# Performance work log

Measured on AMD Instinct MI355X. Metric: run time of the kernel, lower is better.

The kernel has to match this reference:

```python
import jax, jax.numpy as jnp
import numpy as np
import math

HID, NH, NKV, HD = 2048, 16, 4, 128
GROUPS = NH // NKV

def fq(x, bits, axis=None):
    # symmetric fake-quant with straight-through rounding; per-tensor unless axis given
    qmax = 2.0 ** (bits - 1) - 1.0
    if axis is None:
        amax = jnp.max(jnp.abs(x))
    else:
        amax = jnp.max(jnp.abs(x), axis=axis, keepdims=True)
    scale = jnp.maximum(amax, 1e-8) / qmax
    q = jnp.clip(jnp.round(x / scale), -qmax - 1.0, qmax) * scale
    return x + jax.lax.stop_gradient(q - x)

def dyn_quant_linear(x, W, b, w_bits=8):
    # DynamicQuantLinear: per-out-channel weight fake-quant + dynamic per-tensor 8-bit act quant
    Wq = fq(W, w_bits, axis=1)          # W: [out, in]
    xq = fq(x, 8)
    y = xq @ Wq.T
    return y + b if b is not None else y

def fq_matmul(a, b, a_bits, b_bits):
    # FakeQuantMatmul
    return jnp.einsum('hqd,hdk->hqk', fq(a, a_bits), fq(b, b_bits))

def rotate_half(x):
    x1, x2 = jnp.split(x, 2, axis=-1)
    return jnp.concatenate([-x2, x1], axis=-1)

def setup_inputs() -> dict:
    key = jax.random.key(0)
    ks = jax.random.split(key, 12)
    inp = {
        'hidden_states': jax.random.normal(ks[0], (1, 512, HID), jnp.float32),
        'cos': jax.random.uniform(ks[1], (1, 512, HD), jnp.float32),
        'sin': jax.random.uniform(ks[2], (1, 512, HD), jnp.float32),
        'cache_k': jax.random.normal(ks[3], (NKV, 8192, HD), jnp.float32),
        'cache_v': jax.random.normal(ks[4], (NKV, 8192, HD), jnp.float32),
        'mask': jnp.zeros((1, 512, 8192), jnp.float32),
        'Wq': jax.random.normal(ks[5], (NH * HD, HID), jnp.float32) * 0.02,
        'bq': jnp.zeros((NH * HD,), jnp.float32),
        'Wk': jax.random.normal(ks[6], (NKV * HD, HID), jnp.float32) * 0.02,
        'bk': jnp.zeros((NKV * HD,), jnp.float32),
        'Wv': jax.random.normal(ks[7], (NKV * HD, HID), jnp.float32) * 0.02,
        'bv': jnp.zeros((NKV * HD,), jnp.float32),
        'Wo': jax.random.normal(ks[8], (HID, NH * HD), jnp.float32) * 0.02,
    }
    return inp

def reference(hidden_states, cos, sin, cache_k, cache_v, mask, Wq, bq, Wk, bk, Wv, bv, Wo):
    # ConstFakeQuant on incoming caches
    cache_k = fq(cache_k, 8)
    cache_v = fq(cache_v, 8)
    seqlen = hidden_states.shape[1]
    x = hidden_states.reshape(seqlen, HID)  # batch_size == 1
    q = dyn_quant_linear(x, Wq, bq).reshape(seqlen, NH, HD).transpose(1, 0, 2)    # [NH,S,D]
    k = dyn_quant_linear(x, Wk, bk).reshape(seqlen, NKV, HD).transpose(1, 0, 2)   # [NKV,S,D]
    v = dyn_quant_linear(x, Wv, bv).reshape(seqlen, NKV, HD).transpose(1, 0, 2)   # [NKV,S,D]
    # RoPE
    q = q * cos + rotate_half(q) * sin
    k = k * cos + rotate_half(k) * sin
    c_len = cache_k.shape[1]
    # sliding KV cache: drop oldest seqlen, append new
    cache_k = jnp.concatenate([cache_k[:, seqlen:, :], k], axis=1)   # [NKV,c_len,D]
    cache_v = jnp.concatenate([cache_v[:, seqlen:, :], v], axis=1)
    kT = cache_k.transpose(0, 2, 1)                                   # [NKV,D,c_len]
    q4 = q.reshape(NKV, GROUPS * seqlen, HD)
    attn = fq_matmul(q4, kT, 8, 8)                                    # [NKV,G*S,c_len]
    attn = attn.reshape(NH, seqlen, c_len) / math.sqrt(HD)
    attn = attn + mask
    attn = jax.nn.softmax(attn, axis=-1)
    attn = attn.reshape(NKV, GROUPS * seqlen, c_len)
    out = fq_matmul(attn, cache_v, 8, 8)                              # sv: [NKV,G*S,D]
    out = out.reshape(NH, seqlen, HD).transpose(1, 0, 2).reshape(1, seqlen, HID)
    out = dyn_quant_linear(out.reshape(seqlen, HID), Wo, None).reshape(1, seqlen, HID)
    # cache outputs re-fake-quantized
    k_out = fq(k, 8)
    v_out = fq(v, 8)
    return (out, k_out, v_out)
```

## Files before the change

kernel.cpp:

```cpp
#include <hip/hip_runtime.h>
#include <math.h>

#define S_LEN 512
#define HID 2048
#define NH 16
#define NKV 4
#define HD 128
#define CL 8192
#define TAILN (CL - S_LEN)
#define NKO (NKV * S_LEN * HD)
#define KS1 16
#define KCH1 (CL / KS1)
#define KS2 4
#define KCH2 (CL / KS2)
#define INV_SQRT_HD 0.08838834764831845f

typedef unsigned short u16;
typedef __attribute__((ext_vector_type(8))) unsigned short u16x8;
typedef __attribute__((ext_vector_type(4))) unsigned short u16x4;
typedef __attribute__((ext_vector_type(8))) short bf16x8;
typedef __attribute__((ext_vector_type(4))) float f32x4;

enum {
  SC_AMAX_X = 0, SC_AMAX_CK, SC_AMAX_CK_TAIL, SC_AMAX_CV, SC_AMAX_CV_TAIL,
  SC_AMAX_Q, SC_AMAX_K, SC_AMAX_V, SC_AMAX_AO, SC_MIN_L,
  SC_NUM
};

__device__ __forceinline__ float warpMax64(float v) {
  #pragma unroll
  for (int o = 32; o; o >>= 1) v = fmaxf(v, __shfl_down(v, o, 64));
  return v;
}
__device__ __forceinline__ float warpMin64(float v) {
  #pragma unroll
  for (int o = 32; o; o >>= 1) v = fminf(v, __shfl_down(v, o, 64));
  return v;
}
__device__ __forceinline__ float blockMax256(float v) {
  __shared__ float sm_[4];
  __syncthreads();
  v = warpMax64(v);
  if ((threadIdx.x & 63) == 0) sm_[threadIdx.x >> 6] = v;
  __syncthreads();
  return fmaxf(fmaxf(sm_[0], sm_[1]), fmaxf(sm_[2], sm_[3]));
}
__device__ __forceinline__ float blockMin256(float v) {
  __shared__ float sn_[4];
  __syncthreads();
  v = warpMin64(v);
  if ((threadIdx.x & 63) == 0) sn_[threadIdx.x >> 6] = v;
  __syncthreads();
  return fminf(fminf(sn_[0], sn_[1]), fminf(sn_[2], sn_[3]));
}
__device__ __forceinline__ void atomicMinPosF(float* a, float v) {
  atomicMin((unsigned int*)a, __float_as_uint(v));
}
__device__ __forceinline__ float clampq(float q) {
  return fminf(fmaxf(q, -128.f), 127.f);
}
__device__ __forceinline__ u16 bf16bits(float f) {
  return (u16)(__float_as_uint(f) >> 16);
}
__device__ __forceinline__ float mk_scale(float am) {
  return fmaxf(am, 1e-8f) / 127.f;
}
__device__ __forceinline__ void gl2lds16(const u16* g, u16* l) {
  __builtin_amdgcn_global_load_lds((const __attribute__((address_space(1))) void*)g,
                                   (__attribute__((address_space(3))) void*)l, 16, 0, 0);
}

__global__ __launch_bounds__(256) void k_pre(const float* __restrict__ hidden,
                                             const float* __restrict__ ck, const float* __restrict__ cv,
                                             float* __restrict__ pp) {
  int b = blockIdx.x, tid = threadIdx.x;
  if (b < 512) {
    const int n4 = S_LEN * HID / 4;
    float m = 0.f;
    const float4* x4 = (const float4*)hidden;
    for (int i = b * 256 + tid; i < n4; i += 512 * 256) {
      float4 v = x4[i];
      m = fmaxf(m, fmaxf(fmaxf(fabsf(v.x), fabsf(v.y)), fmaxf(fabsf(v.z), fabsf(v.w))));
    }
    m = blockMax256(m);
    if (tid == 0) pp[b] = m;
  } else {
    int isv = b >= 1024;
    int bb = b - (isv ? 1024 : 512);
    const float4* x4 = (const float4*)(isv ? cv : ck);
    const int n4 = NKV * CL * HD / 4;
    float mf = 0.f, mt = 0.f;
    for (int i = bb * 256 + tid; i < n4; i += 512 * 256) {
      float4 v = x4[i];
      float a = fmaxf(fmaxf(fabsf(v.x), fabsf(v.y)), fmaxf(fabsf(v.z), fabsf(v.w)));
      mf = fmaxf(mf, a);
      int t = (i >> 5) & (CL - 1);
      if (t >= S_LEN) mt = fmaxf(mt, a);
    }
    mf = blockMax256(mf);
    mt = blockMax256(mt);
    if (tid == 0) {
      pp[512 + isv * 1024 + bb] = mf;
      pp[1024 + isv * 1024 + bb] = mt;
    }
  }
}

__global__ __launch_bounds__(256) void k_reduce_pre(const float* __restrict__ pp, float* __restrict__ sc) {
  const int slots[5] = {SC_AMAX_X, SC_AMAX_CK, SC_AMAX_CK_TAIL, SC_AMAX_CV, SC_AMAX_CV_TAIL};
  if (threadIdx.x == 0) sc[SC_MIN_L] = INFINITY;
  #pragma unroll
  for (int r = 0; r < 5; r++) {
    float v = fmaxf(pp[r * 512 + threadIdx.x], pp[r * 512 + 256 + threadIdx.x]);
    v = blockMax256(v);
    if (threadIdx.x == 0) sc[slots[r]] = v;
  }
}

__global__ __launch_bounds__(256) void k_quant_w_all(const float* __restrict__ Wq, const float* __restrict__ Wk,
                                                     const float* __restrict__ Wv, const float* __restrict__ Wo,
                                                     u16* __restrict__ WQb, u16* __restrict__ WKb,
                                                     u16* __restrict__ WVb, u16* __restrict__ WOb,
                                                     float* __restrict__ SWq, float* __restrict__ SWk,
                                                     float* __restrict__ SWv, float* __restrict__ SWo) {
  int r = blockIdx.x;
  const float* W; u16* Wb; float* SW; int row;
  if (r < 2048)      { W = Wq; Wb = WQb; SW = SWq; row = r; }
  else if (r < 2560) { W = Wk; Wb = WKb; SW = SWk; row = r - 2048; }
  else if (r < 3072) { W = Wv; Wb = WVb; SW = SWv; row = r - 2560; }
  else               { W = Wo; Wb = WOb; SW = SWo; row = r - 3072; }
  size_t base = (size_t)row * HID;
  const float4* w4 = (const float4*)(W + base);
  int tid = threadIdx.x;
  float4 va = w4[tid];
  float4 vb = w4[tid + 256];
  float am = fmaxf(fmaxf(fmaxf(fabsf(va.x), fabsf(va.y)), fmaxf(fabsf(va.z), fabsf(va.w))),
                   fmaxf(fmaxf(fabsf(vb.x), fabsf(vb.y)), fmaxf(fabsf(vb.z), fabsf(vb.w))));
  am = blockMax256(am);
  float s = fmaxf(am, 1e-8f) / 127.f;
  if (tid == 0) SW[row] = s;
  u16x4 oa, ob;
  oa[0] = bf16bits(clampq(rintf(va.x / s)));
  oa[1] = bf16bits(clampq(rintf(va.y / s)));
  oa[2] = bf16bits(clampq(rintf(va.z / s)));
  oa[3] = bf16bits(clampq(rintf(va.w / s)));
  ob[0] = bf16bits(clampq(rintf(vb.x / s)));
  ob[1] = bf16bits(clampq(rintf(vb.y / s)));
  ob[2] = bf16bits(clampq(rintf(vb.z / s)));
  ob[3] = bf16bits(clampq(rintf(vb.w / s)));
  *(u16x4*)(Wb + base + (size_t)tid * 4) = oa;
  *(u16x4*)(Wb + base + (size_t)(tid + 256) * 4) = ob;
}

__global__ __launch_bounds__(256) void k_quant_act_b(const float* __restrict__ in, u16* __restrict__ outp,
                                                     int n4, const float* __restrict__ sc, int axslot) {
  float s = mk_scale(sc[axslot]);
  const float4* i4 = (const float4*)in;
  for (int i = blockIdx.x * 256 + threadIdx.x; i < n4; i += gridDim.x * 256) {
    float4 v = i4[i];
    u16x4 o;
    o[0] = bf16bits(clampq(rintf(v.x / s)));
    o[1] = bf16bits(clampq(rintf(v.y / s)));
    o[2] = bf16bits(clampq(rintf(v.z / s)));
    o[3] = bf16bits(clampq(rintf(v.w / s)));
    *(u16x4*)(outp + (size_t)i * 4) = o;
  }
}

__global__ __launch_bounds__(256) void k_quant_q(const float* __restrict__ QB, u16* __restrict__ QI,
                                                 const float* __restrict__ sc) {
  int idx = blockIdx.x * 256 + threadIdx.x;
  float s = mk_scale(sc[SC_AMAX_Q]);
  int e = idx * 4;
  int srow = e >> 11, rem = e & 2047;
  int h = rem >> 7, d = rem & 127;
  float4 v = *(const float4*)&QB[e];
  u16x4 o;
  o[0] = bf16bits(clampq(rintf(v.x / s)));
  o[1] = bf16bits(clampq(rintf(v.y / s)));
  o[2] = bf16bits(clampq(rintf(v.z / s)));
  o[3] = bf16bits(clampq(rintf(v.w / s)));
  *(u16x4*)(QI + ((size_t)h * S_LEN + srow) * HD + d) = o;
}

#define GQ_STAGE(BUF, K0)                                                          \
  {                                                                                \
    _Pragma("unroll")                                                              \
    for (int i = 0; i < 2; i++) {                                                  \
      int b = tid + i * 256;                                                       \
      int row = b >> 3, c8d = b & 7, c8s = c8d ^ (row & 7);                        \
      gl2lds16(A + (size_t)(r0 + row) * HID + (K0) + c8s * 8, Al[BUF] + b * 8);    \
    }                                                                              \
    _Pragma("unroll")                                                              \
    for (int i = 0; i < 2; i++) {                                                  \
      int b = tid + i * 256;                                                       \
      int row = b >> 3, c8d = b & 7, c8s = c8d ^ (row & 7);                        \
      gl2lds16(B + (size_t)(c0 + row) * HID + (K0) + c8s * 8, Bl[BUF] + b * 8);    \
    }                                                                              \
  }

#define GQ_TILE(BUF)                                                               \
  {                                                                                \
    _Pragma("unroll")                                                              \
    for (int ks = 0; ks < 2; ks++) {                                               \
      bf16x8 af[2], bfr[2];                                                        \
      _Pragma("unroll")                                                            \
      for (int a = 0; a < 2; a++) {                                                \
        int row = wy * 32 + a * 16 + c;                                            \
        af[a] = *(const bf16x8*)(Al[BUF] + row * 64 + (((4 * ks + g) ^ (row & 7)) * 8)); \
      }                                                                            \
      _Pragma("unroll")                                                            \
      for (int b2 = 0; b2 < 2; b2++) {                                             \
        int row = wx * 32 + b2 * 16 + c;                                           \
        bfr[b2] = *(const bf16x8*)(Bl[BUF] + row * 64 + (((4 * ks + g) ^ (row & 7)) * 8)); \
      }                                                                            \
      _Pragma("unroll")                                                            \
      for (int a = 0; a < 2; a++)                                                  \
        _Pragma("unroll")                                                          \
        for (int b2 = 0; b2 < 2; b2++)                                             \
          acc[a][b2] = __builtin_amdgcn_mfma_f32_16x16x32_bf16(af[a], bfr[b2], acc[a][b2], 0, 0, 0); \
    }                                                                              \
  }

__global__ __launch_bounds__(256) void k_gemm_qkv(const u16* __restrict__ A,
                                                  const u16* __restrict__ WQb, const u16* __restrict__ WKb,
                                                  const u16* __restrict__ WVb,
                                                  const float* __restrict__ SWq, const float* __restrict__ SWk,
                                                  const float* __restrict__ SWv,
                                                  const float* __restrict__ bq, const float* __restrict__ bk,
                                                  const float* __restrict__ bv,
                                                  const float* __restrict__ sc,
                                                  float* __restrict__ QB, float* __restrict__ KB,
                                                  float* __restrict__ VB) {
  __shared__ u16 Al[2][64 * 64];
  __shared__ u16 Bl[2][64 * 64];
  int bx = blockIdx.x;
  const u16* B; const float* SW; const float* bias; float* C; int N, c0;
  if (bx < 32)      { B = WQb; SW = SWq; bias = bq; C = QB; N = HID; c0 = bx * 64; }
  else if (bx < 40) { B = WKb; SW = SWk; bias = bk; C = KB; N = NKV * HD; c0 = (bx - 32) * 64; }
  else              { B = WVb; SW = SWv; bias = bv; C = VB; N = NKV * HD; c0 = (bx - 40) * 64; }
  int tid = threadIdx.x, lane = tid & 63, w = tid >> 6;
  int g = lane >> 4, c = lane & 15;
  int wy = w >> 1, wx = w & 1;
  int r0 = blockIdx.y * 64;
  float sx = mk_scale(sc[SC_AMAX_X]);
  f32x4 acc[2][2] = {};
  GQ_STAGE(0, 0)
  __syncthreads();
  for (int k0 = 0; k0 < HID; k0 += 128) {
    GQ_STAGE(1, k0 + 64)
    GQ_TILE(0)
    __syncthreads();
    if (k0 + 128 < HID) GQ_STAGE(0, k0 + 128)
    GQ_TILE(1)
    __syncthreads();
  }
  #pragma unroll
  for (int a = 0; a < 2; a++)
    #pragma unroll
    for (int b2 = 0; b2 < 2; b2++) {
      int col = c0 + wx * 32 + b2 * 16 + c;
      float sca = sx * SW[col];
      float bs = bias[col];
      #pragma unroll
      for (int r = 0; r < 4; r++) {
        int row = r0 + wy * 32 + a * 16 + 4 * g + r;
        C[(size_t)row * N + col] = acc[a][b2][r] * sca + bs;
      }
    }
}

__global__ __launch_bounds__(256) void k_gemm_q(const u16* __restrict__ A, const u16* __restrict__ B,
                                                const float* __restrict__ SW, const float* __restrict__ sc,
                                                int axslot, float* __restrict__ C, int M, int N, int K) {
  __shared__ u16 Al[2][64 * 64];
  __shared__ u16 Bl[2][64 * 64];
  int tid = threadIdx.x, lane = tid & 63, w = tid >> 6;
  int g = lane >> 4, c = lane & 15;
  int wy = w >> 1, wx = w & 1;
  int r0 = blockIdx.y * 64, c0 = blockIdx.x * 64;
  float sx = mk_scale(sc[axslot]);
  f32x4 acc[2][2] = {};
  GQ_STAGE(0, 0)
  __syncthreads();
  for (int k0 = 0; k0 < HID; k0 += 128) {
    GQ_STAGE(1, k0 + 64)
    GQ_TILE(0)
    __syncthreads();
    if (k0 + 128 < HID) GQ_STAGE(0, k0 + 128)
    GQ_TILE(1)
    __syncthreads();
  }
  #pragma unroll
  for (int a = 0; a < 2; a++)
    #pragma unroll
    for (int b2 = 0; b2 < 2; b2++) {
      int col = c0 + wx * 32 + b2 * 16 + c;
      float sca = sx * SW[col];
      #pragma unroll
      for (int r = 0; r < 4; r++) {
        int row = r0 + wy * 32 + a * 16 + 4 * g + r;
        C[(size_t)row * N + col] = acc[a][b2][r] * sca;
      }
    }
}

__global__ __launch_bounds__(256) void k_rope_amax(float* __restrict__ QB, float* __restrict__ KB,
                                                   const float* __restrict__ VB,
                                                   const float* __restrict__ cosb, const float* __restrict__ sinb,
                                                   float* __restrict__ PR) {
  const int nQ = S_LEN * NH * 64;
  const int nK = S_LEN * NKV * 64;
  int idx = blockIdx.x * 256 + threadIdx.x;
  float am = 0.f;
  if (idx < nQ) {
    int s = idx >> 10, rem = idx & 1023, h = rem >> 6, d = rem & 63;
    float c1 = cosb[s * HD + d], s1 = sinb[s * HD + d];
    float c2 = cosb[s * HD + d + 64], s2 = sinb[s * HD + d + 64];
    float* p = &QB[(size_t)s * (NH * HD) + h * HD + d];
    float x1 = p[0], x2 = p[64];
    float y1 = x1 * c1 - x2 * s1;
    float y2 = x2 * c2 + x1 * s2;
    p[0] = y1; p[64] = y2;
    am = fmaxf(fabsf(y1), fabsf(y2));
  } else if (idx < nQ + nK) {
    int j = idx - nQ;
    int s = j >> 8, rem = j & 255, h = rem >> 6, d = rem & 63;
    float c1 = cosb[s * HD + d], s1 = sinb[s * HD + d];
    float c2 = cosb[s * HD + d + 64], s2 = sinb[s * HD + d + 64];
    float* p = &KB[(size_t)s * (NKV * HD) + h * HD + d];
    float x1 = p[0], x2 = p[64];
    float y1 = x1 * c1 - x2 * s1;
    float y2 = x2 * c2 + x1 * s2;
    p[0] = y1; p[64] = y2;
    am = fmaxf(fabsf(y1), fabsf(y2));
  } else {
    int j = idx - nQ - nK;
    float4 v = ((const float4*)VB)[j];
    am = fmaxf(fmaxf(fabsf(v.x), fabsf(v.y)), fmaxf(fabsf(v.z), fabsf(v.w)));
  }
  am = blockMax256(am);
  if (threadIdx.x == 0) PR[blockIdx.x] = am;
}

__global__ __launch_bounds__(256) void k_reduce_rope(const float* __restrict__ PR, float* __restrict__ sc) {
  float v = 0.f;
  #pragma unroll
  for (int i = 0; i < 8; i++) v = fmaxf(v, PR[threadIdx.x + 256 * i]);
  v = blockMax256(v);
  if (threadIdx.x == 0) sc[SC_AMAX_Q] = v;
  v = fmaxf(PR[2048 + threadIdx.x], PR[2048 + 256 + threadIdx.x]);
  v = blockMax256(v);
  if (threadIdx.x == 0) sc[SC_AMAX_K] = v;
  v = PR[2560 + threadIdx.x];
  v = blockMax256(v);
  if (threadIdx.x == 0) sc[SC_AMAX_V] = v;
}

__global__ __launch_bounds__(256) void k_build_cache2(const float* __restrict__ ck, const float* __restrict__ cv,
                                                      const float* __restrict__ KB, const float* __restrict__ VB,
                                                      u16* __restrict__ KCb, u16* __restrict__ VCb,
                                                      u16* __restrict__ VT, float* __restrict__ dout,
                                                      const float* __restrict__ sc) {
  __shared__ u16 T[64][140];
  int b = blockIdx.x;
  int isv = b >= NKV * 128;
  int bb = b - isv * NKV * 128;
  int kvh = bb >> 7, tb = bb & 127;
  float s1 = mk_scale(sc[isv ? SC_AMAX_CV : SC_AMAX_CK]);
  float tq = fminf(rintf(sc[isv ? SC_AMAX_CV_TAIL : SC_AMAX_CK_TAIL] / s1), 127.f) * s1;
  float s2 = fmaxf(fmaxf(tq, sc[isv ? SC_AMAX_V : SC_AMAX_K]), 1e-8f) / 127.f;
  float so = mk_scale(sc[isv ? SC_AMAX_V : SC_AMAX_K]);
  const float* cache = isv ? cv : ck;
  const float* fresh = isv ? VB : KB;
  u16* Cb = isv ? VCb : KCb;
  int tid = threadIdx.x;
  int t0 = tb * 64;
  #pragma unroll
  for (int i = 0; i < 8; i++) {
    int idx = tid + i * 256;
    int t = idx >> 5, d4 = (idx & 31) << 2;
    int tt = t0 + t;
    float4 x;
    float q0_, q1_, q2_, q3_;
    if (tt < TAILN) {
      x = *(const float4*)&cache[((size_t)kvh * CL + tt + S_LEN) * HD + d4];
      q0_ = clampq(rintf(clampq(rintf(x.x / s1)) * s1 / s2));
      q1_ = clampq(rintf(clampq(rintf(x.y / s1)) * s1 / s2));
      q2_ = clampq(rintf(clampq(rintf(x.z / s1)) * s1 / s2));
      q3_ = clampq(rintf(clampq(rintf(x.w / s1)) * s1 / s2));
    } else {
      x = *(const float4*)&fresh[(size_t)(tt - TAILN) * (NKV * HD) + kvh * HD + d4];
      q0_ = clampq(rintf(x.x / s2));
      q1_ = clampq(rintf(x.y / s2));
      q2_ = clampq(rintf(x.z / s2));
      q3_ = clampq(rintf(x.w / s2));
      float4 o;
      o.x = clampq(rintf(x.x / so)) * so;
      o.y = clampq(rintf(x.y / so)) * so;
      o.z = clampq(rintf(x.z / so)) * so;
      o.w = clampq(rintf(x.w / so)) * so;
      *(float4*)&dout[(size_t)S_LEN * HID + (size_t)isv * NKO +
                      ((size_t)kvh * S_LEN + (tt - TAILN)) * HD + d4] = o;
    }
    u16x4 ov;
    ov[0] = bf16bits(q0_); ov[1] = bf16bits(q1_); ov[2] = bf16bits(q2_); ov[3] = bf16bits(q3_);
    *(u16x4*)(Cb + ((size_t)kvh * CL + tt) * HD + d4) = ov;
    if (isv) *(u16x4*)&T[t][d4] = ov;
  }
  if (isv) {
    __syncthreads();
    #pragma unroll
    for (int i = 0; i < 4; i++) {
      int j = tid + i * 256;
      int d = j >> 3, tc = (j & 7) << 3;
      u16x8 v;
      #pragma unroll
      for (int k = 0; k < 8; k++) v[k] = T[tc + k][d];
      *(u16x8*)(VT + ((size_t)kvh * HD + d) * CL + t0 + tc) = v;
    }
  }
}

#define M1_STAGE(BUF, KBASE)                                                       \
  {                                                                                \
    const u16* kgt = Kg + (size_t)(KBASE) * HD;                                    \
    _Pragma("unroll")                                                              \
    for (int i = 0; i < 4; i++) {                                                  \
      int b = tid + i * 256;                                                       \
      int row = b >> 4, c8d = b & 15, c8s = c8d ^ (row & 7);                       \
      gl2lds16(kgt + row * HD + c8s * 8, Kl[BUF] + b * 8);                         \
    }                                                                              \
  }

#define M1_TILE(BUF, KBASE)                                                        \
  {                                                                                \
    const int kbase_ = (KBASE);                                                    \
    f32x4 sc4[4];                                                                  \
    _Pragma("unroll")                                                              \
    for (int kf = 0; kf < 4; kf++) {                                               \
      f32x4 s4 = {0.f, 0.f, 0.f, 0.f};                                             \
      int krow = kf * 16 + c;                                                      \
      _Pragma("unroll")                                                            \
      for (int ds = 0; ds < 4; ds++) {                                             \
        bf16x8 kf8 = *(const bf16x8*)(Kl[BUF] + krow * HD + (((4 * ds + g) ^ (krow & 7)) * 8)); \
        s4 = __builtin_amdgcn_mfma_f32_16x16x32_bf16(qf[ds], kf8, s4, 0, 0, 0);    \
      }                                                                            \
      sc4[kf] = s4;                                                                \
    }                                                                              \
    _Pragma("unroll")                                                              \
    for (int r = 0; r < 4; r++) {                                                  \
      float v0 = fmaf(sc4[0][r], sscale, mrb[r * CL + kbase_ + c]);                \
      float v1 = fmaf(sc4[1][r], sscale, mrb[r * CL + kbase_ + 16 + c]);           \
      float v2 = fmaf(sc4[2][r], sscale, mrb[r * CL + kbase_ + 32 + c]);           \
      float v3 = fmaf(sc4[3][r], sscale, mrb[r * CL + kbase_ + 48 + c]);           \
      float tmax = fmaxf(fmaxf(v0, v1), fmaxf(v2, v3));                            \
      float nm = fmaxf(m[r], tmax);                                                \
      float e0 = __expf(v0 - nm), e1 = __expf(v1 - nm);                            \
      float e2 = __expf(v2 - nm), e3 = __expf(v3 - nm);                            \
      float f = __expf(m[r] - nm);                                                 \
      l[r] = fmaf(l[r], f, (e0 + e1) + (e2 + e3));                                 \
      m[r] = nm;                                                                   \
    }                                                                              \
  }

__global__ __launch_bounds__(256) void k_mattn1(const u16* __restrict__ QI, const u16* __restrict__ KCb,
                                                const float* __restrict__ mask, const float* __restrict__ sc,
                                                float* __restrict__ PM, float* __restrict__ PL) {
  __shared__ u16 Kl[2][64 * HD];
  int bid = blockIdx.x;
  int wki = (bid & 7) * (NH * 8 * KS1 / 8) + (bid >> 3);
  int kc = wki >> 7, rem2 = wki & 127, qb = rem2 >> 4, h = rem2 & 15, kv = h >> 2;
  int tid = threadIdx.x, lane = tid & 63, wv = tid >> 6, g = lane >> 4, c = lane & 15;
  float sq  = mk_scale(sc[SC_AMAX_Q]);
  float sck = mk_scale(sc[SC_AMAX_CK]);
  float tqk = fminf(rintf(sc[SC_AMAX_CK_TAIL] / sck), 127.f) * sck;
  float skn = fmaxf(fmaxf(tqk, sc[SC_AMAX_K]), 1e-8f) / 127.f;
  float sscale = sq * skn * INV_SQRT_HD;
  int q0 = qb * 64 + wv * 16;
  bf16x8 qf[4];
  {
    const u16* qrow = QI + ((size_t)h * S_LEN + q0 + c) * HD + g * 8;
    #pragma unroll
    for (int ds = 0; ds < 4; ds++) qf[ds] = *(const bf16x8*)(qrow + 32 * ds);
  }
  float m[4], l[4];
  #pragma unroll
  for (int r = 0; r < 4; r++) { m[r] = -INFINITY; l[r] = 0.f; }
  int qlane = q0 + 4 * g;
  int kbase0 = kc * KCH1;
  const u16* Kg = KCb + (size_t)kv * CL * HD;
  const float* mrb = mask + (size_t)qlane * CL;
  M1_STAGE(0, kbase0)
  __syncthreads();
  for (int kb = 0; kb < KCH1; kb += 128) {
    M1_STAGE(1, kbase0 + kb + 64)
    M1_TILE(0, kbase0 + kb)
    __syncthreads();
    if (kb + 128 < KCH1) M1_STAGE(0, kbase0 + kb + 128)
    M1_TILE(1, kbase0 + kb + 64)
    __syncthreads();
  }
  #pragma unroll
  for (int r = 0; r < 4; r++) {
    #pragma unroll
    for (int off = 1; off < 16; off <<= 1) {
      float om = __shfl_xor(m[r], off, 64);
      float ol = __shfl_xor(l[r], off, 64);
      float nm = fmaxf(m[r], om);
      l[r] = l[r] * __expf(m[r] - nm) + ol * __expf(om - nm);
      m[r] = nm;
    }
  }
  if (c == 0) {
    size_t base = ((size_t)kc * NH + h) * S_LEN + qlane;
    #pragma unroll
    for (int r = 0; r < 4; r++) { PM[base + r] = m[r]; PL[base + r] = l[r]; }
  }
}

__global__ __launch_bounds__(256) void k_merge4(const float* __restrict__ PM, const float* __restrict__ PL,
                                                float* __restrict__ MLm, float* __restrict__ MLl, float* sc) {
  int idx = blockIdx.x * 256 + threadIdx.x;
  const int st = NH * S_LEN;
  float m = PM[idx];
  #pragma unroll
  for (int p = 1; p < KS1; p++) m = fmaxf(m, PM[p * st + idx]);
  float l = 0.f;
  #pragma unroll
  for (int p = 0; p < KS1; p++) l += PL[p * st + idx] * __expf(PM[p * st + idx] - m);
  MLm[idx] = m; MLl[idx] = l;
  float lm = blockMin256(l);
  if (threadIdx.x == 0) atomicMinPosF(&sc[SC_MIN_L], lm);
}

#define M2_STAGE(BUF, KBASE)                                                       \
  {                                                                                \
    const u16* kgt = Kg + (size_t)(KBASE) * HD;                                    \
    const u16* vgt = Vg + (KBASE);                                                 \
    _Pragma("unroll")                                                              \
    for (int i = 0; i < 4; i++) {                                                  \
      int b = tid + i * 256;                                                       \
      int row = b >> 4, c8d = b & 15, c8s = c8d ^ (row & 7);                       \
      gl2lds16(kgt + row * HD + c8s * 8, Kl[BUF] + b * 8);                         \
    }                                                                              \
    _Pragma("unroll")                                                              \
    for (int i = 0; i < 4; i++) {                                                  \
      int b = tid + i * 256;                                                       \
      int row = b >> 3, c8d = b & 7, c8s = c8d ^ (row & 7);                        \
      gl2lds16(vgt + (size_t)row * CL + c8s * 8, Vl[BUF] + b * 8);                 \
    }                                                                              \
  }

#define M2_TILE(BUF, KBASE)                                                        \
  {                                                                                \
    const int kbase_ = (KBASE);                                                    \
    _Pragma("unroll")                                                              \
    for (int kf = 0; kf < 4; kf++) {                                               \
      f32x4 s4 = {0.f, 0.f, 0.f, 0.f};                                             \
      int krow = kf * 16 + c;                                                      \
      _Pragma("unroll")                                                            \
      for (int ds = 0; ds < 4; ds++) {                                             \
        bf16x8 kf8 = *(const bf16x8*)(Kl[BUF] + krow * HD + (((4 * ds + g) ^ (krow & 7)) * 8)); \
        s4 = __builtin_amdgcn_mfma_f32_16x16x32_bf16(qf[ds], kf8, s4, 0, 0, 0);    \
      }                                                                            \
      _Pragma("unroll")                                                            \
      for (int r = 0; r < 4; r++) {                                                \
        float v = fmaf(s4[r], sscale, mrb[r * CL + kbase_ + kf * 16 + c]);         \
        float pi = fminf(rintf(__expf(v - mreg[r]) * cvl[r]), 127.f);              \
        int prow = 4 * g + r, pcol = kf * 16 + c;                                  \
        Pw[prow * 64 + (pcol ^ ((prow & 7) << 3))] = bf16bits(pi);                 \
      }                                                                            \
    }                                                                              \
    asm volatile("s_waitcnt lgkmcnt(0)" ::: "memory");                             \
    __builtin_amdgcn_sched_barrier(0);                                             \
    bf16x8 pa0 = *(const bf16x8*)(Pw + c * 64 + ((8 * g) ^ ((c & 7) << 3)));       \
    bf16x8 pa1 = *(const bf16x8*)(Pw + c * 64 + ((32 + 8 * g) ^ ((c & 7) << 3)));  \
    _Pragma("unroll")                                                              \
    for (int dt = 0; dt < 8; dt++) {                                               \
      int drow = dt * 16 + c;                                                      \
      bf16x8 vf0 = *(const bf16x8*)(Vl[BUF] + drow * 64 + ((g ^ (drow & 7)) * 8)); \
      acc[dt] = __builtin_amdgcn_mfma_f32_16x16x32_bf16(pa0, vf0, acc[dt], 0, 0, 0); \
      bf16x8 vf1 = *(const bf16x8*)(Vl[BUF] + drow * 64 + (((4 + g) ^ (drow & 7)) * 8)); \
      acc[dt] = __builtin_amdgcn_mfma_f32_16x16x32_bf16(pa1, vf1, acc[dt], 0, 0, 0); \
    }                                                                              \
  }

__global__ __launch_bounds__(256) void k_mattn2(const u16* __restrict__ QI, const u16* __restrict__ KCb,
                                                const u16* __restrict__ VT, const float* __restrict__ mask,
                                                const float* __restrict__ sc, const float* __restrict__ MLm,
                                                const float* __restrict__ MLl, float* __restrict__ AOp) {
  __shared__ u16 Kl[2][64 * HD];
  __shared__ u16 Vl[2][HD * 64];
  __shared__ u16 Pl[4 * 16 * 64];
  int bid = blockIdx.x;
  int wki = (bid & 7) * (NH * 8 * KS2 / 8) + (bid >> 3);
  int kc = wki >> 7, rem2 = wki & 127, qb = rem2 >> 4, h = rem2 & 15, kv = h >> 2;
  int tid = threadIdx.x, lane = tid & 63, wv = tid >> 6, g = lane >> 4, c = lane & 15;
  float sq  = mk_scale(sc[SC_AMAX_Q]);
  float sck = mk_scale(sc[SC_AMAX_CK]);
  float tqk = fminf(rintf(sc[SC_AMAX_CK_TAIL] / sck), 127.f) * sck;
  float skn = fmaxf(fmaxf(tqk, sc[SC_AMAX_K]), 1e-8f) / 127.f;
  float sscale = sq * skn * INV_SQRT_HD;
  float scv = mk_scale(sc[SC_AMAX_CV]);
  float tqv = fminf(rintf(sc[SC_AMAX_CV_TAIL] / scv), 127.f) * scv;
  float svn = fmaxf(fmaxf(tqv, sc[SC_AMAX_V]), 1e-8f) / 127.f;
  float sp  = mk_scale(1.0f / sc[SC_MIN_L]);
  float rsp = 1.0f / sp;
  float psv = sp * svn;
  int q0 = qb * 64 + wv * 16;
  bf16x8 qf[4];
  {
    const u16* qrow = QI + ((size_t)h * S_LEN + q0 + c) * HD + g * 8;
    #pragma unroll
    for (int ds = 0; ds < 4; ds++) qf[ds] = *(const bf16x8*)(qrow + 32 * ds);
  }
  int qlane = q0 + 4 * g;
  float mreg[4], cvl[4];
  #pragma unroll
  for (int r = 0; r < 4; r++) {
    mreg[r] = MLm[h * S_LEN + qlane + r];
    cvl[r] = rsp / MLl[h * S_LEN + qlane + r];
  }
  f32x4 acc[8] = {};
  const u16* Kg = KCb + (size_t)kv * CL * HD;
  const u16* Vg = VT + (size_t)kv * HD * CL;
  const float* mrb = mask + (size_t)qlane * CL;
  int kbase0 = kc * KCH2;
  u16* Pw = Pl + wv * 1024;
  M2_STAGE(0, kbase0)
  __syncthreads();
  for (int kb = 0; kb < KCH2; kb += 128) {
    M2_STAGE(1, kbase0 + kb + 64)
    M2_TILE(0, kbase0 + kb)
    __syncthreads();
    if (kb + 128 < KCH2) M2_STAGE(0, kbase0 + kb + 128)
    M2_TILE(1, kbase0 + kb + 64)
    __syncthreads();
  }
  float* outp = AOp + (size_t)kc * S_LEN * HID;
  #pragma unroll
  for (int dt = 0; dt < 8; dt++)
    #pragma unroll
    for (int r = 0; r < 4; r++)
      outp[(size_t)(qlane + r) * HID + h * HD + dt * 16 + c] = acc[dt][r] * psv;
}

__global__ __launch_bounds__(256) void k_combine_ao(const float* __restrict__ AOp, float* __restrict__ AO,
                                                    float* __restrict__ PA) {
  int idx = blockIdx.x * 256 + threadIdx.x;
  const int st = S_LEN * HID / 4;
  const f32x4* p4 = (const f32x4*)AOp;
  f32x4 a = p4[idx];
  #pragma unroll
  for (int p = 1; p < KS2; p++) {
    f32x4 b = p4[p * st + idx];
    a = a + b;
  }
  *((f32x4*)AO + idx) = a;
  float am = fmaxf(fmaxf(fabsf(a[0]), fabsf(a[1])), fmaxf(fabsf(a[2]), fabsf(a[3])));
  am = blockMax256(am);
  if (threadIdx.x == 0) PA[blockIdx.x] = am;
}

__global__ __launch_bounds__(256) void k_reduce_ao(const float* __restrict__ PA, float* __restrict__ sc) {
  float v = 0.f;
  #pragma unroll
  for (int i = 0; i < 4; i++) v = fmaxf(v, PA[threadIdx.x + 256 * i]);
  v = blockMax256(v);
  if (threadIdx.x == 0) sc[SC_AMAX_AO] = v;
}

extern "C" void kernel_launch(void* const* d_in, const int* in_sizes, int n_in,
                              void* d_out, int out_size, void* d_ws, size_t ws_size,
                              hipStream_t stream) {
  const float* hidden = (const float*)d_in[0];
  const float* cosb   = (const float*)d_in[1];
  const float* sinb   = (const float*)d_in[2];
  const float* cachek = (const float*)d_in[3];
  const float* cachev = (const float*)d_in[4];
  const float* mask   = (const float*)d_in[5];
  const float* Wq     = (const float*)d_in[6];
  const float* bq     = (const float*)d_in[7];
  const float* Wk     = (const float*)d_in[8];
  const float* bk     = (const float*)d_in[9];
  const float* Wv     = (const float*)d_in[10];
  const float* bv     = (const float*)d_in[11];
  const float* Wo     = (const float*)d_in[12];
  float* out = (float*)d_out;

  char* base = (char*)d_ws;
  auto alloc = [&](size_t bytes) { char* p = base; base += (bytes + 255) & ~(size_t)255; return p; };

  float* SC  = (float*)alloc(64 * 4);
  float* PP  = (float*)alloc(2560 * 4);
  float* PR  = (float*)alloc(2816 * 4);
  float* PA  = (float*)alloc(1024 * 4);
  float* SWq = (float*)alloc(HID * 4);
  float* SWk = (float*)alloc(NKV * HD * 4);
  float* SWv = (float*)alloc(NKV * HD * 4);
  float* SWo = (float*)alloc(HID * 4);
  u16* XI    = (u16*)alloc((size_t)S_LEN * HID * 2);
  u16* WQb   = (u16*)alloc((size_t)HID * HID * 2);
  u16* WKb   = (u16*)alloc((size_t)NKV * HD * HID * 2);
  u16* WVb   = (u16*)alloc((size_t)NKV * HD * HID * 2);
  u16* WOb   = (u16*)alloc((size_t)HID * HID * 2);
  float* QB  = (float*)alloc((size_t)S_LEN * HID * 4);
  float* KB  = (float*)alloc((size_t)S_LEN * NKV * HD * 4);
  float* VB  = (float*)alloc((size_t)S_LEN * NKV * HD * 4);
  u16* KCb   = (u16*)alloc((size_t)NKV * CL * HD * 2);
  u16* VCb   = (u16*)alloc((size_t)NKV * CL * HD * 2);
  u16* VT    = (u16*)alloc((size_t)NKV * HD * CL * 2);
  u16* QI    = (u16*)alloc((size_t)NH * S_LEN * HD * 2);
  float* PM  = (float*)alloc((size_t)KS1 * NH * S_LEN * 4);
  float* PL  = (float*)alloc((size_t)KS1 * NH * S_LEN * 4);
  float* MLm = (float*)alloc((size_t)NH * S_LEN * 4);
  float* MLl = (float*)alloc((size_t)NH * S_LEN * 4);
  float* AOp = (float*)alloc((size_t)KS2 * S_LEN * HID * 4);
  float* AO  = (float*)alloc((size_t)S_LEN * HID * 4);
  u16* AOi   = (u16*)alloc((size_t)S_LEN * HID * 2);

  k_pre<<<1536, 256, 0, stream>>>(hidden, cachek, cachev, PP);
  k_reduce_pre<<<1, 256, 0, stream>>>(PP, SC);
  k_quant_w_all<<<5120, 256, 0, stream>>>(Wq, Wk, Wv, Wo, WQb, WKb, WVb, WOb, SWq, SWk, SWv, SWo);
  k_quant_act_b<<<1024, 256, 0, stream>>>(hidden, XI, S_LEN * HID / 4, SC, SC_AMAX_X);
  {
    dim3 g(48, S_LEN / 64);
    k_gemm_qkv<<<g, 256, 0, stream>>>(XI, WQb, WKb, WVb, SWq, SWk, SWv, bq, bk, bv, SC, QB, KB, VB);
  }
  k_rope_amax<<<2816, 256, 0, stream>>>(QB, KB, VB, cosb, sinb, PR);
  k_reduce_rope<<<1, 256, 0, stream>>>(PR, SC);
  k_build_cache2<<<NKV * 128 * 2, 256, 0, stream>>>(cachek, cachev, KB, VB, KCb, VCb, VT, out, SC);
  k_quant_q<<<1024, 256, 0, stream>>>(QB, QI, SC);
  k_mattn1<<<NH * 8 * KS1, 256, 0, stream>>>(QI, KCb, mask, SC, PM, PL);
  k_merge4<<<NH * S_LEN / 256, 256, 0, stream>>>(PM, PL, MLm, MLl, SC);
  k_mattn2<<<NH * 8 * KS2, 256, 0, stream>>>(QI, KCb, VT, mask, SC, MLm, MLl, AOp);
  k_combine_ao<<<1024, 256, 0, stream>>>(AOp, AO, PA);
  k_reduce_ao<<<1, 256, 0, stream>>>(PA, SC);
  k_quant_act_b<<<1024, 256, 0, stream>>>(AO, AOi, S_LEN * HID / 4, SC, SC_AMAX_AO);
  {
    dim3 g(HID / 64, S_LEN / 64);
    k_gemm_q<<<g, 256, 0, stream>>>(AOi, WOb, SWo, SC, SC_AMAX_AO, out, S_LEN, HID, HID);
  }
  (void)in_sizes; (void)n_in; (void)out_size; (void)ws_size;
}
```

Measured before the change: 211.6 us.

## Compute transposed QK^T in mattn2 and pass P through registers via shuffles

The second attention pass now has each wave handle 32 query rows instead of 16, so every K/V tile loaded into LDS feeds twice as many MFMAs. QK^T is computed with swapped operands so each lane holds consecutive keys for one query, and P is packed and rearranged with cross-lane shuffles instead of a round trip through shared memory. The split over keys goes from 4 to 8 chunks to keep the grid size the same. In exchange the kernel uses more registers, since accumulators double, and the combine kernel reads more partial outputs.

```diff
diff --git a/kernel.cpp b/kernel.cpp
--- a/kernel.cpp
+++ b/kernel.cpp
@@ -11,11 +11,12 @@
 #define NKO (NKV * S_LEN * HD)
 #define KS1 16
 #define KCH1 (CL / KS1)
-#define KS2 4
+#define KS2 8
 #define KCH2 (CL / KS2)
 #define INV_SQRT_HD 0.08838834764831845f
 
 typedef unsigned short u16;
+typedef unsigned int u32;
 typedef __attribute__((ext_vector_type(8))) unsigned short u16x8;
 typedef __attribute__((ext_vector_type(4))) unsigned short u16x4;
 typedef __attribute__((ext_vector_type(8))) short bf16x8;
@@ -555,34 +556,62 @@
 #define M2_TILE(BUF, KBASE)                                                        \
   {                                                                                \
     const int kbase_ = (KBASE);                                                    \
+    u32 pw[2][2][4];                  \
     _Pragma("unroll")                                                              \
     for (int kf = 0; kf < 4; kf++) {                                               \
-      f32x4 s4 = {0.f, 0.f, 0.f, 0.f};                                             \
+      f32x4 s40 = {0.f, 0.f, 0.f, 0.f}, s41 = {0.f, 0.f, 0.f, 0.f};                \
       int krow = kf * 16 + c;                                                      \
       _Pragma("unroll")                                                            \
       for (int ds = 0; ds < 4; ds++) {                                             \
         bf16x8 kf8 = *(const bf16x8*)(Kl[BUF] + krow * HD + (((4 * ds + g) ^ (krow & 7)) * 8)); \
-        s4 = __builtin_amdgcn_mfma_f32_16x16x32_bf16(qf[ds], kf8, s4, 0, 0, 0);    \
+        s40 = __builtin_amdgcn_mfma_f32_16x16x32_bf16(kf8, qf[0][ds], s40, 0, 0, 0); \
+        s41 = __builtin_amdgcn_mfma_f32_16x16x32_bf16(kf8, qf[1][ds], s41, 0, 0, 0); \
       }                                                                            \
+      int keyb = kbase_ + kf * 16 + 4 * g;                                         \
+      float p0 = fminf(rintf(__expf(fmaf(s40[0], sscale, mrb0[keyb + 0]) - mreg[0]) * cvl[0]), 127.f); \
+      float p1 = fminf(rintf(__expf(fmaf(s40[1], sscale, mrb0[keyb + 1]) - mreg[0]) * cvl[0]), 127.f); \
+      float p2 = fminf(rintf(__expf(fmaf(s40[2], sscale, mrb0[keyb + 2]) - mreg[0]) * cvl[0]), 127.f); \
+      float p3 = fminf(rintf(__expf(fmaf(s40[3], sscale, mrb0[keyb + 3]) - mreg[0]) * cvl[0]), 127.f); \
+      pw[0][0][kf] = (u32)bf16bits(p0) | ((u32)bf16bits(p1) << 16);                \
+      pw[0][1][kf] = (u32)bf16bits(p2) | ((u32)bf16bits(p3) << 16);                \
+      p0 = fminf(rintf(__expf(fmaf(s41[0], sscale, mrb1[keyb + 0]) - mreg[1]) * cvl[1]), 127.f); \
+      p1 = fminf(rintf(__expf(fmaf(s41[1], sscale, mrb1[keyb + 1]) - mreg[1]) * cvl[1]), 127.f); \
+      p2 = fminf(rintf(__expf(fmaf(s41[2], sscale, mrb1[keyb + 2]) - mreg[1]) * cvl[1]), 127.f); \
+      p3 = fminf(rintf(__expf(fmaf(s41[3], sscale, mrb1[keyb + 3]) - mreg[1]) * cvl[1]), 127.f); \
+      pw[1][0][kf] = (u32)bf16bits(p0) | ((u32)bf16bits(p1) << 16);                \
+      pw[1][1][kf] = (u32)bf16bits(p2) | ((u32)bf16bits(p3) << 16);                \
+    }                                                                              \
+    int src0 = ((g & 1) * 2) * 16 + c;                                             \
+    int src1 = src0 + 16;                                                          \
+    int hi = g >> 1;                                                               \
+    bf16x8 pa[2][2];                                                               \
+    _Pragma("unroll")                                                              \
+    for (int s = 0; s < 2; s++) {                                                  \
       _Pragma("unroll")                                                            \
-      for (int r = 0; r < 4; r++) {                                                \
-        float v = fmaf(s4[r], sscale, mrb[r * CL + kbase_ + kf * 16 + c]);         \
-        float pi = fminf(rintf(__expf(v - mreg[r]) * cvl[r]), 127.f);              \
-        int prow = 4 * g + r, pcol = kf * 16 + c;                                  \
-        Pw[prow * 64 + (pcol ^ ((prow & 7) << 3))] = bf16bits(pi);                 \
+      for (int u = 0; u < 2; u++) {                                                \
+        int a0 = __shfl((int)pw[u][0][2 * s], src0, 64);                           \
+        int b0 = __shfl((int)pw[u][0][2 * s + 1], src0, 64);                       \
+        int a1 = __shfl((int)pw[u][1][2 * s], src0, 64);                           \
+        int b1 = __shfl((int)pw[u][1][2 * s + 1], src0, 64);                       \
+        int a2 = __shfl((int)pw[u][0][2 * s], src1, 64);                           \
+        int b2 = __shfl((int)pw[u][0][2 * s + 1], src1, 64);                       \
+        int a3 = __shfl((int)pw[u][1][2 * s], src1, 64);                           \
+        int b3 = __shfl((int)pw[u][1][2 * s + 1], src1, 64);                       \
+        int4 wv4;                                                                  \
+        wv4.x = hi ? b0 : a0; wv4.y = hi ? b1 : a1;                                \
+        wv4.z = hi ? b2 : a2; wv4.w = hi ? b3 : a3;                                \
+        pa[u][s] = *(bf16x8*)&wv4;                                                 \
       }                                                                            \
     }                                                                              \
-    asm volatile("s_waitcnt lgkmcnt(0)" ::: "memory");                             \
-    __builtin_amdgcn_sched_barrier(0);                                             \
-    bf16x8 pa0 = *(const bf16x8*)(Pw + c * 64 + ((8 * g) ^ ((c & 7) << 3)));       \
-    bf16x8 pa1 = *(const bf16x8*)(Pw + c * 64 + ((32 + 8 * g) ^ ((c & 7) << 3)));  \
     _Pragma("unroll")                                                              \
     for (int dt = 0; dt < 8; dt++) {                                               \
       int drow = dt * 16 + c;                                                      \
       bf16x8 vf0 = *(const bf16x8*)(Vl[BUF] + drow * 64 + ((g ^ (drow & 7)) * 8)); \
-      acc[dt] = __builtin_amdgcn_mfma_f32_16x16x32_bf16(pa0, vf0, acc[dt], 0, 0, 0); \
+      acc[0][dt] = __builtin_amdgcn_mfma_f32_16x16x32_bf16(pa[0][0], vf0, acc[0][dt], 0, 0, 0); \
+      acc[1][dt] = __builtin_amdgcn_mfma_f32_16x16x32_bf16(pa[1][0], vf0, acc[1][dt], 0, 0, 0); \
       bf16x8 vf1 = *(const bf16x8*)(Vl[BUF] + drow * 64 + (((4 + g) ^ (drow & 7)) * 8)); \
-      acc[dt] = __builtin_amdgcn_mfma_f32_16x16x32_bf16(pa1, vf1, acc[dt], 0, 0, 0); \
+      acc[0][dt] = __builtin_amdgcn_mfma_f32_16x16x32_bf16(pa[0][1], vf1, acc[0][dt], 0, 0, 0); \
+      acc[1][dt] = __builtin_amdgcn_mfma_f32_16x16x32_bf16(pa[1][1], vf1, acc[1][dt], 0, 0, 0); \
     }                                                                              \
   }
 
@@ -592,10 +621,9 @@
                                                 const float* __restrict__ MLl, float* __restrict__ AOp) {
   __shared__ u16 Kl[2][64 * HD];
   __shared__ u16 Vl[2][HD * 64];
-  __shared__ u16 Pl[4 * 16 * 64];
   int bid = blockIdx.x;
-  int wki = (bid & 7) * (NH * 8 * KS2 / 8) + (bid >> 3);
-  int kc = wki >> 7, rem2 = wki & 127, qb = rem2 >> 4, h = rem2 & 15, kv = h >> 2;
+  int wki = (bid & 7) * (NH * 4 * KS2 / 8) + (bid >> 3);
+  int kc = wki >> 6, rem2 = wki & 63, qb = rem2 >> 4, h = rem2 & 15, kv = h >> 2;
   int tid = threadIdx.x, lane = tid & 63, wv = tid >> 6, g = lane >> 4, c = lane & 15;
   float sq  = mk_scale(sc[SC_AMAX_Q]);
   float sck = mk_scale(sc[SC_AMAX_CK]);
@@ -608,26 +636,26 @@
   float sp  = mk_scale(1.0f / sc[SC_MIN_L]);
   float rsp = 1.0f / sp;
   float psv = sp * svn;
-  int q0 = qb * 64 + wv * 16;
-  bf16x8 qf[4];
-  {
-    const u16* qrow = QI + ((size_t)h * S_LEN + q0 + c) * HD + g * 8;
+  int q0 = qb * 128 + wv * 32;
+  bf16x8 qf[2][4];
+  #pragma unroll
+  for (int u = 0; u < 2; u++) {
+    const u16* qrow = QI + ((size_t)h * S_LEN + q0 + 16 * u + c) * HD + g * 8;
     #pragma unroll
-    for (int ds = 0; ds < 4; ds++) qf[ds] = *(const bf16x8*)(qrow + 32 * ds);
-  }
-  int qlane = q0 + 4 * g;
-  float mreg[4], cvl[4];
-  #pragma unroll
-  for (int r = 0; r < 4; r++) {
-    mreg[r] = MLm[h * S_LEN + qlane + r];
-    cvl[r] = rsp / MLl[h * S_LEN + qlane + r];
-  }
-  f32x4 acc[8] = {};
+    for (int ds = 0; ds < 4; ds++) qf[u][ds] = *(const bf16x8*)(qrow + 32 * ds);
+  }
+  float mreg[2], cvl[2];
+  #pragma unroll
+  for (int u = 0; u < 2; u++) {
+    mreg[u] = MLm[h * S_LEN + q0 + 16 * u + c];
+    cvl[u] = rsp / MLl[h * S_LEN + q0 + 16 * u + c];
+  }
+  const float* mrb0 = mask + (size_t)(q0 + c) * CL;
+  const float* mrb1 = mask + (size_t)(q0 + 16 + c) * CL;
+  f32x4 acc[2][8] = {};
   const u16* Kg = KCb + (size_t)kv * CL * HD;
   const u16* Vg = VT + (size_t)kv * HD * CL;
-  const float* mrb = mask + (size_t)qlane * CL;
   int kbase0 = kc * KCH2;
-  u16* Pw = Pl + wv * 1024;
   M2_STAGE(0, kbase0)
   __syncthreads();
   for (int kb = 0; kb < KCH2; kb += 128) {
@@ -640,10 +668,12 @@
   }
   float* outp = AOp + (size_t)kc * S_LEN * HID;
   #pragma unroll
-  for (int dt = 0; dt < 8; dt++)
+  for (int u = 0; u < 2; u++)
     #pragma unroll
-    for (int r = 0; r < 4; r++)
-      outp[(size_t)(qlane + r) * HID + h * HD + dt * 16 + c] = acc[dt][r] * psv;
+    for (int dt = 0; dt < 8; dt++)
+      #pragma unroll
+      for (int r = 0; r < 4; r++)
+        outp[(size_t)(q0 + 16 * u + 4 * g + r) * HID + h * HD + dt * 16 + c] = acc[u][dt][r] * psv;
 }
 
 __global__ __launch_bounds__(256) void k_combine_ao(const float* __restrict__ AOp, float* __restrict__ AO,
@@ -734,7 +764,7 @@
   k_quant_q<<<1024, 256, 0, stream>>>(QB, QI, SC);
   k_mattn1<<<NH * 8 * KS1, 256, 0, stream>>>(QI, KCb, mask, SC, PM, PL);
   k_merge4<<<NH * S_LEN / 256, 256, 0, stream>>>(PM, PL, MLm, MLl, SC);
-  k_mattn2<<<NH * 8 * KS2, 256, 0, stream>>>(QI, KCb, VT, mask, SC, MLm, MLl, AOp);
+  k_mattn2<<<NH * 4 * KS2, 256, 0, stream>>>(QI, KCb, VT, mask, SC, MLm, MLl, AOp);
   k_combine_ao<<<1024, 256, 0, stream>>>(AOp, AO, PA);
   k_reduce_ao<<<1, 256, 0, stream>>>(PA, SC);
   k_quant_act_b<<<1024, 256, 0, stream>>>(AO, AOi, S_LEN * HID / 4, SC, SC_AMAX_AO);
```

New measurement: 211.2 us. No clear change (-0.2%).
